# Kernel tuning notes

Measured on AMD Instinct MI355X. Metric: run time of the kernel, lower is better.

The kernel has to match this reference:

```python
import jax, jax.numpy as jnp
import numpy as np
from jax import lax

DIM = 64
H1 = 1024
H2 = 1024
BATCH = 32768


def build_masks(dim, h1, h2):
    # Standard MADE masks with identity ordering and deterministic hidden degrees.
    deg_in = np.arange(dim)
    deg_h1 = np.arange(h1) % max(1, dim - 1)
    deg_h2 = np.arange(h2) % max(1, dim - 1)
    deg_out = np.concatenate([np.arange(dim), np.arange(dim)])  # (mu, log_sigma)
    M1 = (deg_h1[None, :] >= deg_in[:, None]).astype(np.float32)   # [dim, h1]
    M2 = (deg_h2[None, :] >= deg_h1[:, None]).astype(np.float32)   # [h1, h2]
    M3 = (deg_out[None, :] > deg_h2[:, None]).astype(np.float32)   # [h2, 2*dim]
    return jnp.asarray(M1), jnp.asarray(M2), jnp.asarray(M3)


def setup_inputs() -> dict:
    key = jax.random.key(0)
    ks = jax.random.split(key, 4)
    scale = 0.02
    u = jax.random.normal(ks[0], (BATCH, DIM), dtype=jnp.float32)
    W1 = jax.random.normal(ks[1], (DIM, H1), dtype=jnp.float32) * scale
    b1 = jnp.zeros((H1,), dtype=jnp.float32)
    W2 = jax.random.normal(ks[2], (H1, H2), dtype=jnp.float32) * scale
    b2 = jnp.zeros((H2,), dtype=jnp.float32)
    W3 = jax.random.normal(ks[3], (H2, 2 * DIM), dtype=jnp.float32) * scale
    b3 = jnp.zeros((2 * DIM,), dtype=jnp.float32)
    return {"u": u, "W1": W1, "b1": b1, "W2": W2, "b2": b2, "W3": W3, "b3": b3}


def reference(u, W1, b1, W2, b2, W3, b3):
    B, dim = u.shape
    M1, M2, M3 = build_masks(dim, W1.shape[1], W2.shape[1])

    def made(x):
        h = jax.nn.relu(x @ (W1 * M1) + b1)
        h = jax.nn.relu(h @ (W2 * M2) + b2)
        out = h @ (W3 * M3) + b3
        return out[:, :dim], out[:, dim:]  # mu, log_sigma

    def step(carry, t):
        x, logd = carry
        mu, log_sigma = made(x)
        x = x.at[:, t].set(u[:, t] * jnp.exp(log_sigma[:, t]) + mu[:, t])
        logd = logd + log_sigma[:, t]
        return (x, logd), None

    x0 = jnp.zeros_like(u)
    logd0 = jnp.zeros((B,), dtype=u.dtype)
    (x, logd), _ = lax.scan(step, (x0, logd0), jnp.arange(dim))
    return x, logd
```

## Files before the change

kernel.cpp:

```cpp
#include <hip/hip_runtime.h>
#include <hip/hip_bf16.h>
#include <stdint.h>

typedef __attribute__((ext_vector_type(8))) short bf16x8;
typedef __attribute__((ext_vector_type(4))) float f32x4;
typedef __attribute__((ext_vector_type(4))) unsigned int u32x4;

#define MFMA __builtin_amdgcn_mfma_f32_16x16x32_bf16

__device__ __forceinline__ ushort f2bf(float v) {
    __hip_bfloat16 b = __float2bfloat16(v);
    return *reinterpret_cast<ushort*>(&b);
}

__global__ void prep_all(const float* __restrict__ W1, const float* __restrict__ W2,
                         const float* __restrict__ W3, const float* __restrict__ b1,
                         const float* __restrict__ b2,
                         ushort* __restrict__ W2f2, ushort* __restrict__ W2g2,
                         ushort* __restrict__ W1f, ushort* __restrict__ W3f,
                         float* __restrict__ b1s2, float* __restrict__ b1e,
                         float* __restrict__ b2s2, float* __restrict__ b2e)
{
    int idx = blockIdx.x * 256 + threadIdx.x;
    if (idx < 63 * 33 * 512) {
        int d = idx / (33 * 512); int rem = idx - d * 33 * 512;
        int kc = rem >> 9, r = rem & 511;
        int lane = r >> 3, e = r & 7;
        int col = lane & 15, s = ((lane >> 4) << 3) + e;
        int hout = d + 63 * col;
        float v = 0.f;
        if (kc < 32) {
            int g = 2 * kc + (s >> 4), m = s & 15;
            if (g <= 62) v = W2[(size_t)(g + 63 * m) * 1024 + hout];
        } else if (s < 16) {
            v = W2[(size_t)(1008 + s) * 1024 + hout];
        }
        W2f2[idx] = f2bf(v);
    }
    if (idx < 16 * 9 * 512) {
        int d = idx / (9 * 512); int rem = idx - d * 9 * 512;
        int j = rem >> 9, r = rem & 511;
        int lane = r >> 3, e = r & 7;
        int col = lane & 15, s = ((lane >> 4) << 3) + e;
        float v = 0.f;
        if (col == 0) {
            int hout = 1008 + d;
            if (j < 8) {
                int g = 2 * j + (s >> 4), m = s & 15;
                if (g <= 62) v = W2[(size_t)(g + 63 * m) * 1024 + hout];
            } else if (s < 16) {
                v = W2[(size_t)(1008 + s) * 1024 + hout];
            }
        }
        W2g2[idx] = f2bf(v);
    }
    if (idx < 63 * 2048) {
        int d = idx >> 11; int rem = idx & 2047;
        int kc2 = rem >> 10, nt = (rem >> 9) & 1, r = rem & 511;
        int lane = r >> 3, e = r & 7;
        int col = lane & 15, k = kc2 * 32 + ((lane >> 4) << 3) + e;
        float v = 0.f;
        if (nt == 0) v = W1[(size_t)k * 1024 + d + 63 * col];
        else if (d < 16 && col == 0) v = W1[(size_t)k * 1024 + 1008 + d];
        W1f[idx] = f2bf(v);
    }
    if (idx < 63 * 8 * 512) {
        int d = idx >> 12; int rem = idx & 4095;
        int cb = rem >> 9, r = rem & 511;
        int lane = r >> 3, e = r & 7;
        int ncol = lane & 15, s = ((lane >> 4) << 3) + e;
        int c = cb * 16 + ncol;
        float v = 0.f;
        if (s < 16) v = W3[(size_t)(d + 63 * s) * 128 + c];
        else if (s == 16 && d < 16) v = W3[(size_t)(1008 + d) * 128 + c];
        W3f[idx] = f2bf(v);
    }
    if (idx < 1008) {
        int d = idx >> 4, m = idx & 15;
        b1s2[idx] = b1[d + 63 * m];
        b2s2[idx] = b2[d + 63 * m];
    }
    if (idx < 16) { b1e[idx] = b1[1008 + idx]; b2e[idx] = b2[1008 + idx]; }
}

template<int CM, bool T2>
__device__ __forceinline__ void phase_b(const char* __restrict__ w2p,
                                        const char* __restrict__ w2gp,
                                        const bf16x8 (&h1f)[33], int lane16,
                                        f32x4& o1, f32x4& o2)
{
    constexpr int N = CM + 1;
    constexpr int PF = (N < 4) ? N : 4;
    bf16x8 bb[4]; bf16x8 gg[4];
    #pragma unroll
    for (int i = 0; i < PF; ++i) {
        int kc = (i < CM) ? i : 32;
        bb[i] = *(const bf16x8*)(w2p + kc * 1024 + lane16);
        if constexpr (T2) gg[i] = *(const bf16x8*)(w2gp + i * 1024 + lane16);
    }
    f32x4 c0 = {0,0,0,0}, c1 = {0,0,0,0}, c2 = {0,0,0,0}, c3 = {0,0,0,0};
    f32x4 g0 = {0,0,0,0}, g1 = {0,0,0,0};
    #pragma unroll
    for (int i = 0; i < N; ++i) {
        int kc = (i < CM) ? i : 32;
        bf16x8 a = h1f[kc];
        bf16x8 b = bb[i & 3];
        if ((i & 3) == 0)      c0 = MFMA(a, b, c0, 0, 0, 0);
        else if ((i & 3) == 1) c1 = MFMA(a, b, c1, 0, 0, 0);
        else if ((i & 3) == 2) c2 = MFMA(a, b, c2, 0, 0, 0);
        else                   c3 = MFMA(a, b, c3, 0, 0, 0);
        if constexpr (T2) {
            bf16x8 g = gg[i & 3];
            if (i & 1) g1 = MFMA(a, g, g1, 0, 0, 0);
            else       g0 = MFMA(a, g, g0, 0, 0, 0);
        }
        if (i + 4 < N) {
            int kn = (i + 4 < CM) ? (i + 4) : 32;
            bb[i & 3] = *(const bf16x8*)(w2p + kn * 1024 + lane16);
            if constexpr (T2) gg[i & 3] = *(const bf16x8*)(w2gp + (i + 4) * 1024 + lane16);
        }
    }
    o1 = (c0 + c1) + (c2 + c3);
    if constexpr (T2) o2 = g0 + g1;
}

__global__ __launch_bounds__(256, 2)
void maf_main(const float* __restrict__ U, const float* __restrict__ b3,
              const ushort* __restrict__ W2f2, const ushort* __restrict__ W2g2,
              const ushort* __restrict__ W1f, const ushort* __restrict__ W3f,
              const float* __restrict__ b1s2, const float* __restrict__ b1e,
              const float* __restrict__ b2s2, const float* __restrict__ b2e,
              float* __restrict__ out)
{
    __shared__ char smem[4*1024 + 4*1024 + 4*1024 + 4*2304 + 4*64];
    const int tid = threadIdx.x;
    const int w = tid >> 6, lane = tid & 63;
    const int r16 = lane & 15, q = lane >> 4;
    const int lane16 = lane << 4;
    char*   stgm = smem + w * 1024;
    char*   stge = smem + 4096 + w * 1024;
    char*   h2s  = smem + 8192 + w * 1024;
    ushort* xbs  = (ushort*)(smem + 12288 + w * 2304);
    float*  lgd  = (float*)(smem + 21504 + w * 64);
    const int grow0 = blockIdx.x * 64 + w * 16;

    {
        u32x4 z = {0u, 0u, 0u, 0u};
        for (int i = lane; i < 64; i += 64) *(u32x4*)(stge + i * 16) = z;
        for (int i = lane; i < 64; i += 64) *(u32x4*)(h2s + i * 16) = z;
        for (int i = lane; i < 576; i += 64) ((uint32_t*)xbs)[i] = 0u;
        if (lane < 16) lgd[lane] = 0.f;
    }

    bf16x8 h1f[33];
    #pragma unroll
    for (int i = 0; i < 33; ++i) h1f[i] = (bf16x8){0,0,0,0,0,0,0,0};

    f32x4 am0={0,0,0,0},am1={0,0,0,0},am2={0,0,0,0},am3={0,0,0,0};
    f32x4 al0={0,0,0,0},al1={0,0,0,0},al2={0,0,0,0},al3={0,0,0,0};

    for (int t = 0; t < 64; ++t) {
        const int tt = t >> 4, oc = t & 15;
        const float b3mu = b3[t], b3ls = b3[64 + t];
        float uu[4] = {0.f, 0.f, 0.f, 0.f};
        if (r16 == oc) {
            #pragma unroll
            for (int e = 0; e < 4; ++e)
                uu[e] = U[(size_t)(grow0 + q * 4 + e) * 64 + t];
        }

        if (t > 0) {
            const int d = t - 1;
            const int jc = d >> 1;

            {
                const char* w1p = (const char*)W1f + (size_t)d * 4096 + lane16;
                bf16x8 wf00 = *(const bf16x8*)(w1p);
                bf16x8 wf10 = *(const bf16x8*)(w1p + 2048);
                bf16x8 xa0 = *(const bf16x8*)(xbs + r16 * 72 + q * 8);
                bf16x8 xa1 = *(const bf16x8*)(xbs + r16 * 72 + 32 + q * 8);
                f32x4 h = {0,0,0,0};
                h = MFMA(xa0, wf00, h, 0, 0, 0);
                h = MFMA(xa1, wf10, h, 0, 0, 0);
                float bb1 = b1s2[d * 16 + r16];
                #pragma unroll
                for (int e = 0; e < 4; ++e) {
                    int row = q * 4 + e;
                    ushort hv = f2bf(fmaxf(h[e] + bb1, 0.f));
                    *(ushort*)(stgm + ((row * 64 + ((d & 1) << 5) + r16 * 2) ^ ((row & 3) << 4))) = hv;
                    if (!(d & 1))
                        *(ushort*)(stgm + ((row * 64 + 32 + r16 * 2) ^ ((row & 3) << 4))) = 0;
                }
                if (d < 16) {
                    bf16x8 wf01 = *(const bf16x8*)(w1p + 1024);
                    bf16x8 wf11 = *(const bf16x8*)(w1p + 3072);
                    f32x4 g = {0,0,0,0};
                    g = MFMA(xa0, wf01, g, 0, 0, 0);
                    g = MFMA(xa1, wf11, g, 0, 0, 0);
                    if (r16 == 0) {
                        float be = b1e[d];
                        #pragma unroll
                        for (int e = 0; e < 4; ++e) {
                            int row = q * 4 + e;
                            ushort hv = f2bf(fmaxf(g[e] + be, 0.f));
                            *(ushort*)(stge + ((row * 64 + d * 2) ^ ((row & 3) << 4))) = hv;
                        }
                    }
                }
            }
            {
                bf16x8 nf = *(const bf16x8*)(stgm + ((r16 * 64 + q * 16) ^ ((r16 & 3) << 4)));
                switch (jc) {
                    case 0:  h1f[0]=nf;  break; case 1:  h1f[1]=nf;  break;
                    case 2:  h1f[2]=nf;  break; case 3:  h1f[3]=nf;  break;
                    case 4:  h1f[4]=nf;  break; case 5:  h1f[5]=nf;  break;
                    case 6:  h1f[6]=nf;  break; case 7:  h1f[7]=nf;  break;
                    case 8:  h1f[8]=nf;  break; case 9:  h1f[9]=nf;  break;
                    case 10: h1f[10]=nf; break; case 11: h1f[11]=nf; break;
                    case 12: h1f[12]=nf; break; case 13: h1f[13]=nf; break;
                    case 14: h1f[14]=nf; break; case 15: h1f[15]=nf; break;
                    case 16: h1f[16]=nf; break; case 17: h1f[17]=nf; break;
                    case 18: h1f[18]=nf; break; case 19: h1f[19]=nf; break;
                    case 20: h1f[20]=nf; break; case 21: h1f[21]=nf; break;
                    case 22: h1f[22]=nf; break; case 23: h1f[23]=nf; break;
                    case 24: h1f[24]=nf; break; case 25: h1f[25]=nf; break;
                    case 26: h1f[26]=nf; break; case 27: h1f[27]=nf; break;
                    case 28: h1f[28]=nf; break; case 29: h1f[29]=nf; break;
                    case 30: h1f[30]=nf; break; default: h1f[31]=nf; break;
                }
                if (d < 16)
                    h1f[32] = *(const bf16x8*)(stge + ((r16 * 64 + q * 16) ^ ((r16 & 3) << 4)));
            }

            f32x4 o1, o2 = {0,0,0,0};
            const char* w2p = (const char*)W2f2 + (size_t)d * 33 * 1024;
            const char* w2gp = (const char*)W2g2 + (size_t)d * 9 * 1024;
            if (t <= 16)      phase_b<8,  true >(w2p, w2gp, h1f, lane16, o1, o2);
            else if (t <= 28) phase_b<14, false>(w2p, w2gp, h1f, lane16, o1, o2);
            else if (t <= 40) phase_b<20, false>(w2p, w2gp, h1f, lane16, o1, o2);
            else if (t <= 52) phase_b<26, false>(w2p, w2gp, h1f, lane16, o1, o2);
            else              phase_b<32, false>(w2p, w2gp, h1f, lane16, o1, o2);

            {
                const char* w3p = (const char*)W3f + (size_t)d * 8192 + lane16;
                bf16x8 f0 = *(const bf16x8*)(w3p);
                bf16x8 f1 = *(const bf16x8*)(w3p + 1024);
                bf16x8 f2 = *(const bf16x8*)(w3p + 2048);
                bf16x8 f3 = *(const bf16x8*)(w3p + 3072);
                bf16x8 f4 = *(const bf16x8*)(w3p + 4096);
                bf16x8 f5 = *(const bf16x8*)(w3p + 5120);
                bf16x8 f6 = *(const bf16x8*)(w3p + 6144);
                bf16x8 f7 = *(const bf16x8*)(w3p + 7168);
                float bb2 = b2s2[d * 16 + r16];
                #pragma unroll
                for (int e = 0; e < 4; ++e) {
                    int row = q * 4 + e;
                    ushort hv = f2bf(fmaxf(o1[e] + bb2, 0.f));
                    *(ushort*)(h2s + ((row * 64 + r16 * 2) ^ ((row & 3) << 4))) = hv;
                }
                if (r16 == 0) {
                    float be2 = (d < 16) ? b2e[d] : 0.f;
                    #pragma unroll
                    for (int e = 0; e < 4; ++e) {
                        int row = q * 4 + e;
                        ushort hv = (d < 16) ? f2bf(fmaxf(o2[e] + be2, 0.f)) : (ushort)0;
                        *(ushort*)(h2s + ((row * 64 + 32) ^ ((row & 3) << 4))) = hv;
                    }
                }
                bf16x8 ha = *(const bf16x8*)(h2s + ((r16 * 64 + q * 16) ^ ((r16 & 3) << 4)));
                am0 = MFMA(ha, f0, am0, 0, 0, 0);
                am1 = MFMA(ha, f1, am1, 0, 0, 0);
                am2 = MFMA(ha, f2, am2, 0, 0, 0);
                am3 = MFMA(ha, f3, am3, 0, 0, 0);
                al0 = MFMA(ha, f4, al0, 0, 0, 0);
                al1 = MFMA(ha, f5, al1, 0, 0, 0);
                al2 = MFMA(ha, f6, al2, 0, 0, 0);
                al3 = MFMA(ha, f7, al3, 0, 0, 0);
            }
        }

        {
            f32x4 vm = (tt == 0) ? am0 : (tt == 1) ? am1 : (tt == 2) ? am2 : am3;
            f32x4 vl = (tt == 0) ? al0 : (tt == 1) ? al1 : (tt == 2) ? al2 : al3;
            if (r16 == oc) {
                #pragma unroll
                for (int e = 0; e < 4; ++e) {
                    int row = q * 4 + e;
                    float mu = vm[e] + b3mu;
                    float ls = vl[e] + b3ls;
                    float xv = uu[e] * expf(ls) + mu;
                    out[(size_t)(grow0 + row) * 64 + t] = xv;
                    xbs[row * 72 + t] = f2bf(xv);
                    lgd[row] += ls;
                }
            }
        }
    }

    if (lane < 16) out[(size_t)32768 * 64 + grow0 + lane] = lgd[lane];
}

extern "C" void kernel_launch(void* const* d_in, const int* in_sizes, int n_in,
                              void* d_out, int out_size, void* d_ws, size_t ws_size,
                              hipStream_t stream) {
    const float* U  = (const float*)d_in[0];
    const float* W1 = (const float*)d_in[1];
    const float* b1 = (const float*)d_in[2];
    const float* W2 = (const float*)d_in[3];
    const float* b2 = (const float*)d_in[4];
    const float* W3 = (const float*)d_in[5];
    const float* b3 = (const float*)d_in[6];
    float* out = (float*)d_out;

    char* ws = (char*)d_ws;
    ushort* W2f2 = (ushort*)ws;
    ushort* W2g2 = (ushort*)(ws + 2128896);
    ushort* W1f  = (ushort*)(ws + 2276352);
    ushort* W3f  = (ushort*)(ws + 2534400);
    float*  b1s2 = (float*)(ws + 3050496);
    float*  b1e  = (float*)(ws + 3054592);
    float*  b2s2 = (float*)(ws + 3054720);
    float*  b2e  = (float*)(ws + 3058752);

    prep_all<<<4160, 256, 0, stream>>>(W1, W2, W3, b1, b2,
                                       W2f2, W2g2, W1f, W3f, b1s2, b1e, b2s2, b2e);
    maf_main<<<512, 256, 0, stream>>>(U, b3, W2f2, W2g2, W1f, W3f,
                                      b1s2, b1e, b2s2, b2e, out);
}
```

Baseline: 281.7 us.

## Stage per-step weights into double-buffered LDS via async global-to-LDS DMA

Each wave used to load its W1, W2 and W3 fragments for the current step straight from global memory. Now the eight waves of a block share one copy of those fragments: it is prefetched for the next step with global_load_lds into a double-buffered LDS area, and a waitcnt plus barrier ends each step. Blocks grow to 512 threads with about 135 KB of dynamic LDS, and the W2 slot layout is reordered so the extra slot comes first. This is meant to cut redundant L2/HBM weight traffic and hide load latency, but it adds a block-wide barrier every step and depends on a vmcnt threshold that may not fully cover the DMA completions.

```diff
diff --git a/kernel.cpp b/kernel.cpp
--- a/kernel.cpp
+++ b/kernel.cpp
@@ -7,6 +7,14 @@
 typedef __attribute__((ext_vector_type(4))) unsigned int u32x4;
 
 #define MFMA __builtin_amdgcn_mfma_f32_16x16x32_bf16
+
+#define BUFSZ 46080
+#define W1OFF 33792
+#define W3OFF 37888
+#define SMEM_TOTAL 135680
+
+typedef __attribute__((address_space(3))) unsigned int lds_u32;
+typedef const __attribute__((address_space(1))) unsigned int glb_u32;
 
 __device__ __forceinline__ ushort f2bf(float v) {
     __hip_bfloat16 b = __float2bfloat16(v);
@@ -24,33 +32,27 @@
     int idx = blockIdx.x * 256 + threadIdx.x;
     if (idx < 63 * 33 * 512) {
         int d = idx / (33 * 512); int rem = idx - d * 33 * 512;
-        int kc = rem >> 9, r = rem & 511;
+        int slot = rem >> 9, r = rem & 511;
         int lane = r >> 3, e = r & 7;
         int col = lane & 15, s = ((lane >> 4) << 3) + e;
         int hout = d + 63 * col;
         float v = 0.f;
-        if (kc < 32) {
-            int g = 2 * kc + (s >> 4), m = s & 15;
-            if (g <= 62) v = W2[(size_t)(g + 63 * m) * 1024 + hout];
-        } else if (s < 16) {
-            v = W2[(size_t)(1008 + s) * 1024 + hout];
-        }
+        if (slot == 0) { if (s < 16) v = W2[(size_t)(1008 + s) * 1024 + hout]; }
+        else { int j = slot - 1; int g = 2 * j + (s >> 4), m = s & 15;
+               if (g <= 62) v = W2[(size_t)(g + 63 * m) * 1024 + hout]; }
         W2f2[idx] = f2bf(v);
     }
     if (idx < 16 * 9 * 512) {
         int d = idx / (9 * 512); int rem = idx - d * 9 * 512;
-        int j = rem >> 9, r = rem & 511;
+        int slot = rem >> 9, r = rem & 511;
         int lane = r >> 3, e = r & 7;
         int col = lane & 15, s = ((lane >> 4) << 3) + e;
         float v = 0.f;
         if (col == 0) {
             int hout = 1008 + d;
-            if (j < 8) {
-                int g = 2 * j + (s >> 4), m = s & 15;
-                if (g <= 62) v = W2[(size_t)(g + 63 * m) * 1024 + hout];
-            } else if (s < 16) {
-                v = W2[(size_t)(1008 + s) * 1024 + hout];
-            }
+            if (slot == 0) { if (s < 16) v = W2[(size_t)(1008 + s) * 1024 + hout]; }
+            else { int j = slot - 1; int g = 2 * j + (s >> 4), m = s & 15;
+                   if (g <= 62) v = W2[(size_t)(g + 63 * m) * 1024 + hout]; }
         }
         W2g2[idx] = f2bf(v);
     }
@@ -83,48 +85,54 @@
     if (idx < 16) { b1e[idx] = b1[1008 + idx]; b2e[idx] = b2[1008 + idx]; }
 }
 
-template<int CM, bool T2>
-__device__ __forceinline__ void phase_b(const char* __restrict__ w2p,
-                                        const char* __restrict__ w2gp,
+__device__ __forceinline__ void issue_dma(int tn, int w, int lane16, char* buf,
+                                          const char* W2p, const char* W2gp,
+                                          const char* W1p, const char* W3p)
+{
+    const int d = tn - 1;
+    const int ns = (tn <= 16) ? 9 : (tn <= 28) ? 15 : (tn <= 40) ? 21 : (tn <= 52) ? 27 : 33;
+    const int ng = (tn <= 16) ? 9 : 0;
+    const char* w2s = W2p + (size_t)d * 33 * 1024;
+    const char* w2g = W2gp + (size_t)d * 9 * 1024;
+    const char* w1s = W1p + (size_t)d * 4096;
+    const char* w3s = W3p + (size_t)d * 8192;
+    const int F = ns + ng + 12;
+    for (int f = w; f < F; f += 8) {
+        const char* src; char* dst;
+        if (f < ns)                { src = w2s + f * 1024;             dst = buf + f * 1024; }
+        else if (f < ns + ng)      { int i = f - ns;      src = w2g + i * 1024; dst = buf + (9 + i) * 1024; }
+        else if (f < ns + ng + 4)  { int i = f - ns - ng; src = w1s + i * 1024; dst = buf + W1OFF + i * 1024; }
+        else                       { int i = f - ns - ng - 4; src = w3s + i * 1024; dst = buf + W3OFF + i * 1024; }
+        __builtin_amdgcn_global_load_lds((glb_u32*)(src + lane16), (lds_u32*)dst, 16, 0, 0);
+    }
+}
+
+template<int NS, bool T2>
+__device__ __forceinline__ void phase_b(const char* __restrict__ w2l,
                                         const bf16x8 (&h1f)[33], int lane16,
                                         f32x4& o1, f32x4& o2)
 {
-    constexpr int N = CM + 1;
-    constexpr int PF = (N < 4) ? N : 4;
-    bf16x8 bb[4]; bf16x8 gg[4];
-    #pragma unroll
-    for (int i = 0; i < PF; ++i) {
-        int kc = (i < CM) ? i : 32;
-        bb[i] = *(const bf16x8*)(w2p + kc * 1024 + lane16);
-        if constexpr (T2) gg[i] = *(const bf16x8*)(w2gp + i * 1024 + lane16);
-    }
     f32x4 c0 = {0,0,0,0}, c1 = {0,0,0,0}, c2 = {0,0,0,0}, c3 = {0,0,0,0};
     f32x4 g0 = {0,0,0,0}, g1 = {0,0,0,0};
     #pragma unroll
-    for (int i = 0; i < N; ++i) {
-        int kc = (i < CM) ? i : 32;
-        bf16x8 a = h1f[kc];
-        bf16x8 b = bb[i & 3];
+    for (int i = 0; i < NS; ++i) {
+        bf16x8 b = *(const bf16x8*)(w2l + i * 1024 + lane16);
+        bf16x8 a = h1f[i];
         if ((i & 3) == 0)      c0 = MFMA(a, b, c0, 0, 0, 0);
         else if ((i & 3) == 1) c1 = MFMA(a, b, c1, 0, 0, 0);
         else if ((i & 3) == 2) c2 = MFMA(a, b, c2, 0, 0, 0);
         else                   c3 = MFMA(a, b, c3, 0, 0, 0);
         if constexpr (T2) {
-            bf16x8 g = gg[i & 3];
+            bf16x8 g = *(const bf16x8*)(w2l + (9 + i) * 1024 + lane16);
             if (i & 1) g1 = MFMA(a, g, g1, 0, 0, 0);
             else       g0 = MFMA(a, g, g0, 0, 0, 0);
         }
-        if (i + 4 < N) {
-            int kn = (i + 4 < CM) ? (i + 4) : 32;
-            bb[i & 3] = *(const bf16x8*)(w2p + kn * 1024 + lane16);
-            if constexpr (T2) gg[i & 3] = *(const bf16x8*)(w2gp + (i + 4) * 1024 + lane16);
-        }
     }
     o1 = (c0 + c1) + (c2 + c3);
     if constexpr (T2) o2 = g0 + g1;
 }
 
-__global__ __launch_bounds__(256, 2)
+__global__ __launch_bounds__(512, 2)
 void maf_main(const float* __restrict__ U, const float* __restrict__ b3,
               const ushort* __restrict__ W2f2, const ushort* __restrict__ W2g2,
               const ushort* __restrict__ W1f, const ushort* __restrict__ W3f,
@@ -132,22 +140,23 @@
               const float* __restrict__ b2s2, const float* __restrict__ b2e,
               float* __restrict__ out)
 {
-    __shared__ char smem[4*1024 + 4*1024 + 4*1024 + 4*2304 + 4*64];
+    extern __shared__ char smem[];
     const int tid = threadIdx.x;
     const int w = tid >> 6, lane = tid & 63;
     const int r16 = lane & 15, q = lane >> 4;
     const int lane16 = lane << 4;
-    char*   stgm = smem + w * 1024;
-    char*   stge = smem + 4096 + w * 1024;
-    char*   h2s  = smem + 8192 + w * 1024;
-    ushort* xbs  = (ushort*)(smem + 12288 + w * 2304);
-    float*  lgd  = (float*)(smem + 21504 + w * 64);
-    const int grow0 = blockIdx.x * 64 + w * 16;
+    char*   bufs = smem;
+    char*   stgm = smem + 92160 + w * 1024;
+    char*   stge = smem + 100352 + w * 1024;
+    char*   h2s  = smem + 108544 + w * 1024;
+    ushort* xbs  = (ushort*)(smem + 116736 + w * 2304);
+    float*  lgd  = (float*)(smem + 135168 + w * 64);
+    const int grow0 = blockIdx.x * 128 + w * 16;
 
     {
         u32x4 z = {0u, 0u, 0u, 0u};
-        for (int i = lane; i < 64; i += 64) *(u32x4*)(stge + i * 16) = z;
-        for (int i = lane; i < 64; i += 64) *(u32x4*)(h2s + i * 16) = z;
+        *(u32x4*)(stge + lane * 16) = z;
+        *(u32x4*)(h2s + lane * 16) = z;
         for (int i = lane; i < 576; i += 64) ((uint32_t*)xbs)[i] = 0u;
         if (lane < 16) lgd[lane] = 0.f;
     }
@@ -161,28 +170,39 @@
 
     for (int t = 0; t < 64; ++t) {
         const int tt = t >> 4, oc = t & 15;
+        const int d = t - 1;
+        float uu0=0.f, uu1=0.f, uu2=0.f, uu3=0.f;
+        if (r16 == oc) {
+            const float* up = U + (size_t)(grow0 + q * 4) * 64 + t;
+            uu0 = up[0]; uu1 = up[64]; uu2 = up[128]; uu3 = up[192];
+        }
+        float bb1 = 0.f, bb2 = 0.f, be1 = 0.f, be2 = 0.f;
+        if (t > 0) {
+            bb1 = b1s2[d * 16 + r16];
+            bb2 = b2s2[d * 16 + r16];
+            if (d < 16) { be1 = b1e[d]; be2 = b2e[d]; }
+        }
         const float b3mu = b3[t], b3ls = b3[64 + t];
-        float uu[4] = {0.f, 0.f, 0.f, 0.f};
-        if (r16 == oc) {
-            #pragma unroll
-            for (int e = 0; e < 4; ++e)
-                uu[e] = U[(size_t)(grow0 + q * 4 + e) * 64 + t];
-        }
+
+        if (t < 63)
+            issue_dma(t + 1, w, lane16, bufs + (((t + 1) & 1) * BUFSZ),
+                      (const char*)W2f2, (const char*)W2g2,
+                      (const char*)W1f, (const char*)W3f);
+
+        const char* buf = bufs + ((t & 1) * BUFSZ);
 
         if (t > 0) {
-            const int d = t - 1;
             const int jc = d >> 1;
 
             {
-                const char* w1p = (const char*)W1f + (size_t)d * 4096 + lane16;
-                bf16x8 wf00 = *(const bf16x8*)(w1p);
-                bf16x8 wf10 = *(const bf16x8*)(w1p + 2048);
+                const char* w1l = buf + W1OFF;
+                bf16x8 wf00 = *(const bf16x8*)(w1l + lane16);
+                bf16x8 wf10 = *(const bf16x8*)(w1l + 2048 + lane16);
                 bf16x8 xa0 = *(const bf16x8*)(xbs + r16 * 72 + q * 8);
                 bf16x8 xa1 = *(const bf16x8*)(xbs + r16 * 72 + 32 + q * 8);
                 f32x4 h = {0,0,0,0};
                 h = MFMA(xa0, wf00, h, 0, 0, 0);
                 h = MFMA(xa1, wf10, h, 0, 0, 0);
-                float bb1 = b1s2[d * 16 + r16];
                 #pragma unroll
                 for (int e = 0; e < 4; ++e) {
                     int row = q * 4 + e;
@@ -192,18 +212,17 @@
                         *(ushort*)(stgm + ((row * 64 + 32 + r16 * 2) ^ ((row & 3) << 4))) = 0;
                 }
                 if (d < 16) {
-                    bf16x8 wf01 = *(const bf16x8*)(w1p + 1024);
-                    bf16x8 wf11 = *(const bf16x8*)(w1p + 3072);
+                    bf16x8 wf01 = *(const bf16x8*)(w1l + 1024 + lane16);
+                    bf16x8 wf11 = *(const bf16x8*)(w1l + 3072 + lane16);
                     f32x4 g = {0,0,0,0};
                     g = MFMA(xa0, wf01, g, 0, 0, 0);
                     g = MFMA(xa1, wf11, g, 0, 0, 0);
                     if (r16 == 0) {
-                        float be = b1e[d];
                         #pragma unroll
                         for (int e = 0; e < 4; ++e) {
                             int row = q * 4 + e;
-                            ushort hv = f2bf(fmaxf(g[e] + be, 0.f));
-                            *(ushort*)(stge + ((row * 64 + d * 2) ^ ((row & 3) << 4))) = hv;
+                            *(ushort*)(stge + ((row * 64 + d * 2) ^ ((row & 3) << 4))) =
+                                f2bf(fmaxf(g[e] + be1, 0.f));
                         }
                     }
                 }
@@ -211,47 +230,44 @@
             {
                 bf16x8 nf = *(const bf16x8*)(stgm + ((r16 * 64 + q * 16) ^ ((r16 & 3) << 4)));
                 switch (jc) {
-                    case 0:  h1f[0]=nf;  break; case 1:  h1f[1]=nf;  break;
-                    case 2:  h1f[2]=nf;  break; case 3:  h1f[3]=nf;  break;
-                    case 4:  h1f[4]=nf;  break; case 5:  h1f[5]=nf;  break;
-                    case 6:  h1f[6]=nf;  break; case 7:  h1f[7]=nf;  break;
-                    case 8:  h1f[8]=nf;  break; case 9:  h1f[9]=nf;  break;
-                    case 10: h1f[10]=nf; break; case 11: h1f[11]=nf; break;
-                    case 12: h1f[12]=nf; break; case 13: h1f[13]=nf; break;
-                    case 14: h1f[14]=nf; break; case 15: h1f[15]=nf; break;
-                    case 16: h1f[16]=nf; break; case 17: h1f[17]=nf; break;
-                    case 18: h1f[18]=nf; break; case 19: h1f[19]=nf; break;
-                    case 20: h1f[20]=nf; break; case 21: h1f[21]=nf; break;
-                    case 22: h1f[22]=nf; break; case 23: h1f[23]=nf; break;
-                    case 24: h1f[24]=nf; break; case 25: h1f[25]=nf; break;
-                    case 26: h1f[26]=nf; break; case 27: h1f[27]=nf; break;
-                    case 28: h1f[28]=nf; break; case 29: h1f[29]=nf; break;
-                    case 30: h1f[30]=nf; break; default: h1f[31]=nf; break;
+                    case 0:  h1f[1]=nf;  break; case 1:  h1f[2]=nf;  break;
+                    case 2:  h1f[3]=nf;  break; case 3:  h1f[4]=nf;  break;
+                    case 4:  h1f[5]=nf;  break; case 5:  h1f[6]=nf;  break;
+                    case 6:  h1f[7]=nf;  break; case 7:  h1f[8]=nf;  break;
+                    case 8:  h1f[9]=nf;  break; case 9:  h1f[10]=nf; break;
+                    case 10: h1f[11]=nf; break; case 11: h1f[12]=nf; break;
+                    case 12: h1f[13]=nf; break; case 13: h1f[14]=nf; break;
+                    case 14: h1f[15]=nf; break; case 15: h1f[16]=nf; break;
+                    case 16: h1f[17]=nf; break; case 17: h1f[18]=nf; break;
+                    case 18: h1f[19]=nf; break; case 19: h1f[20]=nf; break;
+                    case 20: h1f[21]=nf; break; case 21: h1f[22]=nf; break;
+                    case 22: h1f[23]=nf; break; case 23: h1f[24]=nf; break;
+                    case 24: h1f[25]=nf; break; case 25: h1f[26]=nf; break;
+                    case 26: h1f[27]=nf; break; case 27: h1f[28]=nf; break;
+                    case 28: h1f[29]=nf; break; case 29: h1f[30]=nf; break;
+                    case 30: h1f[31]=nf; break; default: h1f[32]=nf; break;
                 }
                 if (d < 16)
-                    h1f[32] = *(const bf16x8*)(stge + ((r16 * 64 + q * 16) ^ ((r16 & 3) << 4)));
+                    h1f[0] = *(const bf16x8*)(stge + ((r16 * 64 + q * 16) ^ ((r16 & 3) << 4)));
             }
 
             f32x4 o1, o2 = {0,0,0,0};
-            const char* w2p = (const char*)W2f2 + (size_t)d * 33 * 1024;
-            const char* w2gp = (const char*)W2g2 + (size_t)d * 9 * 1024;
-            if (t <= 16)      phase_b<8,  true >(w2p, w2gp, h1f, lane16, o1, o2);
-            else if (t <= 28) phase_b<14, false>(w2p, w2gp, h1f, lane16, o1, o2);
-            else if (t <= 40) phase_b<20, false>(w2p, w2gp, h1f, lane16, o1, o2);
-            else if (t <= 52) phase_b<26, false>(w2p, w2gp, h1f, lane16, o1, o2);
-            else              phase_b<32, false>(w2p, w2gp, h1f, lane16, o1, o2);
+            if (t <= 16)      phase_b<9,  true >(buf, h1f, lane16, o1, o2);
+            else if (t <= 28) phase_b<15, false>(buf, h1f, lane16, o1, o2);
+            else if (t <= 40) phase_b<21, false>(buf, h1f, lane16, o1, o2);
+            else if (t <= 52) phase_b<27, false>(buf, h1f, lane16, o1, o2);
+            else              phase_b<33, false>(buf, h1f, lane16, o1, o2);
 
             {
-                const char* w3p = (const char*)W3f + (size_t)d * 8192 + lane16;
-                bf16x8 f0 = *(const bf16x8*)(w3p);
-                bf16x8 f1 = *(const bf16x8*)(w3p + 1024);
-                bf16x8 f2 = *(const bf16x8*)(w3p + 2048);
-                bf16x8 f3 = *(const bf16x8*)(w3p + 3072);
-                bf16x8 f4 = *(const bf16x8*)(w3p + 4096);
-                bf16x8 f5 = *(const bf16x8*)(w3p + 5120);
-                bf16x8 f6 = *(const bf16x8*)(w3p + 6144);
-                bf16x8 f7 = *(const bf16x8*)(w3p + 7168);
-                float bb2 = b2s2[d * 16 + r16];
+                const char* w3l = buf + W3OFF;
+                bf16x8 f0 = *(const bf16x8*)(w3l + lane16);
+                bf16x8 f1 = *(const bf16x8*)(w3l + 1024 + lane16);
+                bf16x8 f2 = *(const bf16x8*)(w3l + 2048 + lane16);
+                bf16x8 f3 = *(const bf16x8*)(w3l + 3072 + lane16);
+                bf16x8 f4 = *(const bf16x8*)(w3l + 4096 + lane16);
+                bf16x8 f5 = *(const bf16x8*)(w3l + 5120 + lane16);
+                bf16x8 f6 = *(const bf16x8*)(w3l + 6144 + lane16);
+                bf16x8 f7 = *(const bf16x8*)(w3l + 7168 + lane16);
                 #pragma unroll
                 for (int e = 0; e < 4; ++e) {
                     int row = q * 4 + e;
@@ -259,7 +275,6 @@
                     *(ushort*)(h2s + ((row * 64 + r16 * 2) ^ ((row & 3) << 4))) = hv;
                 }
                 if (r16 == 0) {
-                    float be2 = (d < 16) ? b2e[d] : 0.f;
                     #pragma unroll
                     for (int e = 0; e < 4; ++e) {
                         int row = q * 4 + e;
@@ -283,6 +298,7 @@
             f32x4 vm = (tt == 0) ? am0 : (tt == 1) ? am1 : (tt == 2) ? am2 : am3;
             f32x4 vl = (tt == 0) ? al0 : (tt == 1) ? al1 : (tt == 2) ? al2 : al3;
             if (r16 == oc) {
+                float uu[4] = {uu0, uu1, uu2, uu3};
                 #pragma unroll
                 for (int e = 0; e < 4; ++e) {
                     int row = q * 4 + e;
@@ -295,6 +311,8 @@
                 }
             }
         }
+
+        asm volatile("s_waitcnt vmcnt(4)\n\ts_barrier" ::: "memory");
     }
 
     if (lane < 16) out[(size_t)32768 * 64 + grow0 + lane] = lgd[lane];
@@ -324,6 +342,9 @@
 
     prep_all<<<4160, 256, 0, stream>>>(W1, W2, W3, b1, b2,
                                        W2f2, W2g2, W1f, W3f, b1s2, b1e, b2s2, b2e);
-    maf_main<<<512, 256, 0, stream>>>(U, b3, W2f2, W2g2, W1f, W3f,
-                                      b1s2, b1e, b2s2, b2e, out);
-}
+
+    hipFuncSetAttribute(reinterpret_cast<const void*>(&maf_main),
+                        hipFuncAttributeMaxDynamicSharedMemorySize, SMEM_TOTAL);
+    maf_main<<<256, 512, SMEM_TOTAL, stream>>>(U, b3, W2f2, W2g2, W1f, W3f,
+                                               b1s2, b1e, b2s2, b2e, out);
+}
```

Result: slower. 707.1 us (+151.0%).
